# Performance work log

Measured on AMD Instinct MI355X. Metric: run time of the kernel, lower is better.

Reference implementation:

```python
import jax, jax.numpy as jnp
import numpy as np

N_VOCAB_TOTAL = 32064  # n_vocab + n_nts
D_MODEL = 256


def setup_inputs() -> dict:
    key = jax.random.key(0)
    ks = jax.random.split(key, 8)
    d = D_MODEL
    tokens = jax.random.randint(ks[0], (64, 4095), 0, N_VOCAB_TOTAL, dtype=jnp.int32)
    # embedding_tgt: normal with std 1/sqrt(d) (reset_parameters)
    E = jax.random.normal(ks[1], (N_VOCAB_TOTAL, d), dtype=jnp.float32) / jnp.sqrt(jnp.float32(d))
    s_in = 1.0 / np.sqrt(3 * d)
    s_h = 1.0 / np.sqrt(d)
    W_in = jax.random.uniform(ks[2], (d, 3 * d), jnp.float32, -s_in, s_in)  # Linear(3d, d)
    b_in = jax.random.uniform(ks[3], (d,), jnp.float32, -s_in, s_in)
    W1 = jax.random.uniform(ks[4], (d, d), jnp.float32, -s_h, s_h)
    b1 = jax.random.uniform(ks[5], (d,), jnp.float32, -s_h, s_h)
    W2 = jax.random.uniform(ks[6], (d, d), jnp.float32, -s_h, s_h)
    b2 = jax.random.uniform(ks[7], (d,), jnp.float32, -s_h, s_h)
    return {"tokens": tokens, "E": E, "W_in": W_in, "b_in": b_in,
            "W1": W1, "b1": b1, "W2": W2, "b2": b2}


def _bin_agg(roots, left, right, W_in, b_in, W1, b1, W2, b2):
    # skipmlp_binary_agg: root + hidden(inp(cat([root,left,right])))
    # hidden = ELU -> Linear -> ELU -> Linear  (nlayers=2)
    x = jnp.concatenate([roots, left, right], axis=-1)        # [..., 3d]
    h = x @ W_in.T + b_in                                     # inp: Linear(3d, d)
    h = jax.nn.elu(h) @ W1.T + b1
    h = jax.nn.elu(h) @ W2.T + b2
    return roots + h


def reference(tokens, E, W_in, b_in, W1, b1, W2, b2):
    # tokens: [B, N] heap-ordered perfect binary trees, N = 2^(D+1)-1.
    B, N = tokens.shape
    n_leaves = (N + 1) // 2
    emb = E[tokens]                                           # [B, N, d] gather
    cur = emb[:, N - n_leaves:]                               # leaf level, [B, 2^D, d]
    level = n_leaves // 2
    while level >= 1:                                          # fixed D iterations
        roots = emb[:, level - 1: 2 * level - 1]               # [B, level, d]
        left = cur[:, 0::2]
        right = cur[:, 1::2]
        cur = _bin_agg(roots, left, right, W_in, b_in, W1, b1, W2, b2)
        level //= 2
    return cur[:, 0]                                           # [B, d] root embeddings
```

## Files before the change

kernel.cpp:

```cpp
#include <hip/hip_runtime.h>
#include <stdint.h>


typedef __attribute__((ext_vector_type(8))) short short8;
typedef __attribute__((ext_vector_type(4))) float f32x4;

#define XS_STRIDE 264
#define TOK_N 4095

__device__ __forceinline__ unsigned short f32_to_bf16(float f) {
    union { float f; unsigned u; } v; v.f = f;
    return (unsigned short)((v.u + 0x7fffu + ((v.u >> 16) & 1u)) >> 16);
}
__device__ __forceinline__ float bf16_to_f32(unsigned short u) {
    union { unsigned u; float f; } v; v.u = ((unsigned)u) << 16; return v.f;
}

__global__ void convert_f32_bf16(const float* __restrict__ E,
                                 const float* __restrict__ Win,
                                 const float* __restrict__ W1,
                                 const float* __restrict__ W2,
                                 unsigned short* __restrict__ Ebf,
                                 unsigned short* __restrict__ Winbf,
                                 unsigned short* __restrict__ W1bf,
                                 unsigned short* __restrict__ W2bf) {
    const int nE = 32064 * 256, nWin = 256 * 768, nW = 256 * 256;
    const int total4 = (nE + nWin + 2 * nW) >> 2;
    for (int i = blockIdx.x * blockDim.x + threadIdx.x; i < total4;
         i += gridDim.x * blockDim.x) {
        int idx = i << 2;
        const float* src; unsigned short* dst; int off;
        if (idx < nE)                  { src = E;   dst = Ebf;   off = idx; }
        else if (idx < nE + nWin)      { src = Win; dst = Winbf; off = idx - nE; }
        else if (idx < nE + nWin + nW) { src = W1;  dst = W1bf;  off = idx - nE - nWin; }
        else                           { src = W2;  dst = W2bf;  off = idx - nE - nWin - nW; }
        float4 f = *(const float4*)(src + off);
        ushort4 o;
        o.x = f32_to_bf16(f.x); o.y = f32_to_bf16(f.y);
        o.z = f32_to_bf16(f.z); o.w = f32_to_bf16(f.w);
        *(ushort4*)(dst + off) = o;
    }
}

template<int MT>
__global__ __launch_bounds__(256, 4)
void tree_level(const int* __restrict__ tokens,
                const unsigned short* __restrict__ Ebf,
                const unsigned short* __restrict__ Win,
                const unsigned short* __restrict__ W1,
                const unsigned short* __restrict__ W2,
                const float* __restrict__ b_in,
                const float* __restrict__ b1,
                const float* __restrict__ b2,
                const unsigned short* __restrict__ cur_in,
                unsigned short* __restrict__ cur_out,
                float* __restrict__ final_out,
                int L, int logL, int first, int last)
{
    constexpr int R = MT * 16;
    constexpr int GITER = R / 8;
    __shared__ unsigned short Xs[R * XS_STRIDE];

    const int tid  = threadIdx.x;
    const int lane = tid & 63;
    const int wid  = tid >> 6;
    const int l15  = lane & 15;
    const int q    = lane >> 4;
    const int n0   = wid * 64;
    const int blk  = blockIdx.x;
    const int c    = tid & 31;
    const int sub  = tid >> 5;

    auto gsrc = [&](int p, int r) -> const unsigned short* {
        int g = blk * R + r;
        int b = g >> logL;
        int i = g - (b << logL);
        if (p == 0) {
            int tok = tokens[b * TOK_N + (L - 1) + i];
            return Ebf + (size_t)tok * 256;
        } else if (first) {
            int tok = tokens[b * TOK_N + 2047 + 2 * i + (p - 1)];
            return Ebf + (size_t)tok * 256;
        } else {
            return cur_in + ((size_t)b * (2 * L) + 2 * i + (p - 1)) * 256;
        }
    };

    short8 g[GITER];

#pragma unroll
    for (int it = 0; it < GITER; ++it)
        g[it] = *(const short8*)(gsrc(0, it * 8 + sub) + c * 8);
#pragma unroll
    for (int it = 0; it < GITER; ++it)
        *(short8*)(&Xs[(it * 8 + sub) * XS_STRIDE + c * 8]) = g[it];
    __syncthreads();

    f32x4 acc[MT][4];
    float bv[4];
#pragma unroll
    for (int nt = 0; nt < 4; ++nt) bv[nt] = b_in[n0 + nt * 16 + l15];
#pragma unroll
    for (int mt = 0; mt < MT; ++mt)
#pragma unroll
        for (int nt = 0; nt < 4; ++nt)
            acc[mt][nt] = (f32x4){bv[nt], bv[nt], bv[nt], bv[nt]};

    const unsigned short* wbase = Win + q * 8 + (size_t)(n0 + l15) * 768;
    for (int p = 0; p < 3; ++p) {
        const int kbase = p * 256;
        short8 bb[2][4];
#pragma unroll
        for (int k = 0; k < 2; ++k)
#pragma unroll
            for (int nt = 0; nt < 4; ++nt)
                bb[k][nt] = *(const short8*)(wbase + (size_t)(nt * 16) * 768 + kbase + k * 32);
        if (p < 2) {
#pragma unroll
            for (int it = 0; it < GITER; ++it)
                g[it] = *(const short8*)(gsrc(p + 1, it * 8 + sub) + c * 8);
        }
#pragma unroll
        for (int k = 0; k < 8; ++k) {
            short8 a[MT];
#pragma unroll
            for (int mt = 0; mt < MT; ++mt)
                a[mt] = *(const short8*)(&Xs[(mt * 16 + l15) * XS_STRIDE + k * 32 + q * 8]);
#pragma unroll
            for (int mt = 0; mt < MT; ++mt)
#pragma unroll
                for (int nt = 0; nt < 4; ++nt)
                    acc[mt][nt] = __builtin_amdgcn_mfma_f32_16x16x32_bf16(
                        a[mt], bb[k & 1][nt], acc[mt][nt], 0, 0, 0);
            if (k + 2 < 8) {
#pragma unroll
                for (int nt = 0; nt < 4; ++nt)
                    bb[k & 1][nt] = *(const short8*)(wbase + (size_t)(nt * 16) * 768 + kbase + (k + 2) * 32);
            }
        }
        __syncthreads();
        if (p < 2) {
#pragma unroll
            for (int it = 0; it < GITER; ++it)
                *(short8*)(&Xs[(it * 8 + sub) * XS_STRIDE + c * 8]) = g[it];
            __syncthreads();
        }
    }

#pragma unroll
    for (int mt = 0; mt < MT; ++mt)
#pragma unroll
        for (int nt = 0; nt < 4; ++nt)
#pragma unroll
            for (int r = 0; r < 4; ++r) {
                float h = acc[mt][nt][r];
                h = h > 0.f ? h : (__expf(h) - 1.f);
                Xs[(mt * 16 + q * 4 + r) * XS_STRIDE + n0 + nt * 16 + l15] = f32_to_bf16(h);
            }
    __syncthreads();

#pragma unroll
    for (int nt = 0; nt < 4; ++nt) bv[nt] = b1[n0 + nt * 16 + l15];
#pragma unroll
    for (int mt = 0; mt < MT; ++mt)
#pragma unroll
        for (int nt = 0; nt < 4; ++nt)
            acc[mt][nt] = (f32x4){bv[nt], bv[nt], bv[nt], bv[nt]};
    {
        const unsigned short* w1base = W1 + q * 8 + (size_t)(n0 + l15) * 256;
        short8 bb[2][4];
#pragma unroll
        for (int k = 0; k < 2; ++k)
#pragma unroll
            for (int nt = 0; nt < 4; ++nt)
                bb[k][nt] = *(const short8*)(w1base + (size_t)(nt * 16) * 256 + k * 32);
#pragma unroll
        for (int it = 0; it < GITER; ++it)
            g[it] = *(const short8*)(gsrc(0, it * 8 + sub) + c * 8);
#pragma unroll
        for (int k = 0; k < 8; ++k) {
            short8 a[MT];
#pragma unroll
            for (int mt = 0; mt < MT; ++mt)
                a[mt] = *(const short8*)(&Xs[(mt * 16 + l15) * XS_STRIDE + k * 32 + q * 8]);
#pragma unroll
            for (int mt = 0; mt < MT; ++mt)
#pragma unroll
                for (int nt = 0; nt < 4; ++nt)
                    acc[mt][nt] = __builtin_amdgcn_mfma_f32_16x16x32_bf16(
                        a[mt], bb[k & 1][nt], acc[mt][nt], 0, 0, 0);
            if (k + 2 < 8) {
#pragma unroll
                for (int nt = 0; nt < 4; ++nt)
                    bb[k & 1][nt] = *(const short8*)(w1base + (size_t)(nt * 16) * 256 + (k + 2) * 32);
            }
        }
    }
    __syncthreads();

#pragma unroll
    for (int mt = 0; mt < MT; ++mt)
#pragma unroll
        for (int nt = 0; nt < 4; ++nt)
#pragma unroll
            for (int r = 0; r < 4; ++r) {
                float h = acc[mt][nt][r];
                h = h > 0.f ? h : (__expf(h) - 1.f);
                Xs[(mt * 16 + q * 4 + r) * XS_STRIDE + n0 + nt * 16 + l15] = f32_to_bf16(h);
            }
    __syncthreads();

#pragma unroll
    for (int nt = 0; nt < 4; ++nt) bv[nt] = b2[n0 + nt * 16 + l15];
#pragma unroll
    for (int mt = 0; mt < MT; ++mt)
#pragma unroll
        for (int nt = 0; nt < 4; ++nt)
            acc[mt][nt] = (f32x4){bv[nt], bv[nt], bv[nt], bv[nt]};
    {
        const unsigned short* w2base = W2 + q * 8 + (size_t)(n0 + l15) * 256;
        short8 bb[2][4];
#pragma unroll
        for (int k = 0; k < 2; ++k)
#pragma unroll
            for (int nt = 0; nt < 4; ++nt)
                bb[k][nt] = *(const short8*)(w2base + (size_t)(nt * 16) * 256 + k * 32);
#pragma unroll
        for (int k = 0; k < 8; ++k) {
            short8 a[MT];
#pragma unroll
            for (int mt = 0; mt < MT; ++mt)
                a[mt] = *(const short8*)(&Xs[(mt * 16 + l15) * XS_STRIDE + k * 32 + q * 8]);
#pragma unroll
            for (int mt = 0; mt < MT; ++mt)
#pragma unroll
                for (int nt = 0; nt < 4; ++nt)
                    acc[mt][nt] = __builtin_amdgcn_mfma_f32_16x16x32_bf16(
                        a[mt], bb[k & 1][nt], acc[mt][nt], 0, 0, 0);
            if (k + 2 < 8) {
#pragma unroll
                for (int nt = 0; nt < 4; ++nt)
                    bb[k & 1][nt] = *(const short8*)(w2base + (size_t)(nt * 16) * 256 + (k + 2) * 32);
            }
        }
    }
    __syncthreads();
#pragma unroll
    for (int it = 0; it < GITER; ++it)
        *(short8*)(&Xs[(it * 8 + sub) * XS_STRIDE + c * 8]) = g[it];
    __syncthreads();

#pragma unroll
    for (int mt = 0; mt < MT; ++mt)
#pragma unroll
        for (int r = 0; r < 4; ++r) {
            int row = mt * 16 + q * 4 + r;
            int gg  = blk * R + row;
#pragma unroll
            for (int nt = 0; nt < 4; ++nt) {
                int col = n0 + nt * 16 + l15;
                float o = acc[mt][nt][r] + bf16_to_f32(Xs[row * XS_STRIDE + col]);
                if (last) final_out[(size_t)gg * 256 + col] = o;
                else      cur_out[(size_t)gg * 256 + col] = f32_to_bf16(o);
            }
        }
}

extern "C" void kernel_launch(void* const* d_in, const int* in_sizes, int n_in,
                              void* d_out, int out_size, void* d_ws, size_t ws_size,
                              hipStream_t stream) {
    const int*   tokens = (const int*)  d_in[0];
    const float* E      = (const float*)d_in[1];
    const float* W_in   = (const float*)d_in[2];
    const float* b_in   = (const float*)d_in[3];
    const float* W1     = (const float*)d_in[4];
    const float* b1     = (const float*)d_in[5];
    const float* W2     = (const float*)d_in[6];
    const float* b2     = (const float*)d_in[7];
    float* out = (float*)d_out;
    char* ws = (char*)d_ws;

    unsigned short* Ebf   = (unsigned short*)(ws);
    unsigned short* Winbf = (unsigned short*)(ws + 16416768);
    unsigned short* W1bf  = (unsigned short*)(ws + 16809984);
    unsigned short* W2bf  = (unsigned short*)(ws + 16941056);
    unsigned short* curA  = (unsigned short*)(ws + 17072128);
    unsigned short* curB  = (unsigned short*)(ws + 50626560);

    convert_f32_bf16<<<1024, 256, 0, stream>>>(E, W_in, W1, W2,
                                               Ebf, Winbf, W1bf, W2bf);

    const unsigned short* cin = curA;
    unsigned short* cout = curA;
    int first = 1;
    for (int L = 1024; L >= 1; L >>= 1) {
        int logL = 31 - __builtin_clz((unsigned)L);
        int last = (L == 1);
        int MTs = (L >= 512) ? 4 : (L == 256 ? 2 : 1);
        int blocks = (64 * L) / (16 * MTs);
        if (MTs == 4)
            tree_level<4><<<dim3(blocks), dim3(256), 0, stream>>>(
                tokens, Ebf, Winbf, W1bf, W2bf, b_in, b1, b2,
                cin, last ? nullptr : cout, last ? out : nullptr, L, logL, first, last);
        else if (MTs == 2)
            tree_level<2><<<dim3(blocks), dim3(256), 0, stream>>>(
                tokens, Ebf, Winbf, W1bf, W2bf, b_in, b1, b2,
                cin, last ? nullptr : cout, last ? out : nullptr, L, logL, first, last);
        else
            tree_level<1><<<dim3(blocks), dim3(256), 0, stream>>>(
                tokens, Ebf, Winbf, W1bf, W2bf, b_in, b1, b2,
                cin, last ? nullptr : cout, last ? out : nullptr, L, logL, first, last);
        cin = cout;
        cout = (cout == curA) ? curB : curA;
        first = 0;
    }
}
```

Before: 530.7 us.

## Fuse small tree levels into one per-batch tail kernel and refactor GEMM passes

Levels 32 down to 1 now run in a single persistent kernel with one block per batch tree, keeping the previous level in shared memory instead of issuing six tiny launches that round-trip through global memory. The GEMM inner loop moves into a shared helper with a deeper weight prefetch for small tiles, and the next gather is scheduled late inside the K loop. Output writes are staged through shared memory so stores to global are coalesced, and launch bounds drop to 3 blocks per SM. The tail kernel runs only 64 blocks and wastes MFMA work on padded rows when levels are small, so it may leave much of the GPU idle.

```diff
diff --git a/kernel.cpp b/kernel.cpp
--- a/kernel.cpp
+++ b/kernel.cpp
@@ -42,8 +42,41 @@
     }
 }
 
+template<int MT, int DEPTH, int WROW, typename F>
+__device__ __forceinline__ void run_pass(const unsigned short* __restrict__ Xs,
+                                         const unsigned short* __restrict__ wlane,
+                                         int kbase, f32x4 (&acc)[MT][4],
+                                         int l15, int q, F&& late)
+{
+    short8 bb[DEPTH][4];
+#pragma unroll
+    for (int d = 0; d < DEPTH; ++d)
+#pragma unroll
+        for (int nt = 0; nt < 4; ++nt)
+            bb[d][nt] = *(const short8*)(wlane + (size_t)(nt * 16) * WROW + kbase + d * 32);
+#pragma unroll
+    for (int k = 0; k < 8; ++k) {
+        if (k == 6) { __builtin_amdgcn_sched_barrier(0); late(); }
+        short8 a[MT];
+#pragma unroll
+        for (int mt = 0; mt < MT; ++mt)
+            a[mt] = *(const short8*)(&Xs[(mt * 16 + l15) * XS_STRIDE + k * 32 + q * 8]);
+#pragma unroll
+        for (int mt = 0; mt < MT; ++mt)
+#pragma unroll
+            for (int nt = 0; nt < 4; ++nt)
+                acc[mt][nt] = __builtin_amdgcn_mfma_f32_16x16x32_bf16(
+                    a[mt], bb[k % DEPTH][nt], acc[mt][nt], 0, 0, 0);
+        if (k + DEPTH < 8) {
+#pragma unroll
+            for (int nt = 0; nt < 4; ++nt)
+                bb[k % DEPTH][nt] = *(const short8*)(wlane + (size_t)(nt * 16) * WROW + kbase + (k + DEPTH) * 32);
+        }
+    }
+}
+
 template<int MT>
-__global__ __launch_bounds__(256, 4)
+__global__ __launch_bounds__(256, 3)
 void tree_level(const int* __restrict__ tokens,
                 const unsigned short* __restrict__ Ebf,
                 const unsigned short* __restrict__ Win,
@@ -54,11 +87,11 @@
                 const float* __restrict__ b2,
                 const unsigned short* __restrict__ cur_in,
                 unsigned short* __restrict__ cur_out,
-                float* __restrict__ final_out,
-                int L, int logL, int first, int last)
+                int L, int logL, int first)
 {
     constexpr int R = MT * 16;
     constexpr int GITER = R / 8;
+    constexpr int DEPTH = (MT >= 4) ? 2 : 4;
     __shared__ unsigned short Xs[R * XS_STRIDE];
 
     const int tid  = threadIdx.x;
@@ -106,38 +139,15 @@
         for (int nt = 0; nt < 4; ++nt)
             acc[mt][nt] = (f32x4){bv[nt], bv[nt], bv[nt], bv[nt]};
 
-    const unsigned short* wbase = Win + q * 8 + (size_t)(n0 + l15) * 768;
+    const unsigned short* winlane = Win + q * 8 + (size_t)(n0 + l15) * 768;
     for (int p = 0; p < 3; ++p) {
-        const int kbase = p * 256;
-        short8 bb[2][4];
-#pragma unroll
-        for (int k = 0; k < 2; ++k)
-#pragma unroll
-            for (int nt = 0; nt < 4; ++nt)
-                bb[k][nt] = *(const short8*)(wbase + (size_t)(nt * 16) * 768 + kbase + k * 32);
-        if (p < 2) {
-#pragma unroll
-            for (int it = 0; it < GITER; ++it)
-                g[it] = *(const short8*)(gsrc(p + 1, it * 8 + sub) + c * 8);
-        }
-#pragma unroll
-        for (int k = 0; k < 8; ++k) {
-            short8 a[MT];
-#pragma unroll
-            for (int mt = 0; mt < MT; ++mt)
-                a[mt] = *(const short8*)(&Xs[(mt * 16 + l15) * XS_STRIDE + k * 32 + q * 8]);
-#pragma unroll
-            for (int mt = 0; mt < MT; ++mt)
-#pragma unroll
-                for (int nt = 0; nt < 4; ++nt)
-                    acc[mt][nt] = __builtin_amdgcn_mfma_f32_16x16x32_bf16(
-                        a[mt], bb[k & 1][nt], acc[mt][nt], 0, 0, 0);
-            if (k + 2 < 8) {
-#pragma unroll
-                for (int nt = 0; nt < 4; ++nt)
-                    bb[k & 1][nt] = *(const short8*)(wbase + (size_t)(nt * 16) * 768 + kbase + (k + 2) * 32);
+        run_pass<MT, DEPTH, 768>(Xs, winlane, p * 256, acc, l15, q, [&]() {
+            if (p < 2) {
+#pragma unroll
+                for (int it = 0; it < GITER; ++it)
+                    g[it] = *(const short8*)(gsrc(p + 1, it * 8 + sub) + c * 8);
             }
-        }
+        });
         __syncthreads();
         if (p < 2) {
 #pragma unroll
@@ -166,36 +176,8 @@
 #pragma unroll
         for (int nt = 0; nt < 4; ++nt)
             acc[mt][nt] = (f32x4){bv[nt], bv[nt], bv[nt], bv[nt]};
-    {
-        const unsigned short* w1base = W1 + q * 8 + (size_t)(n0 + l15) * 256;
-        short8 bb[2][4];
-#pragma unroll
-        for (int k = 0; k < 2; ++k)
-#pragma unroll
-            for (int nt = 0; nt < 4; ++nt)
-                bb[k][nt] = *(const short8*)(w1base + (size_t)(nt * 16) * 256 + k * 32);
-#pragma unroll
-        for (int it = 0; it < GITER; ++it)
-            g[it] = *(const short8*)(gsrc(0, it * 8 + sub) + c * 8);
-#pragma unroll
-        for (int k = 0; k < 8; ++k) {
-            short8 a[MT];
-#pragma unroll
-            for (int mt = 0; mt < MT; ++mt)
-                a[mt] = *(const short8*)(&Xs[(mt * 16 + l15) * XS_STRIDE + k * 32 + q * 8]);
-#pragma unroll
-            for (int mt = 0; mt < MT; ++mt)
-#pragma unroll
-                for (int nt = 0; nt < 4; ++nt)
-                    acc[mt][nt] = __builtin_amdgcn_mfma_f32_16x16x32_bf16(
-                        a[mt], bb[k & 1][nt], acc[mt][nt], 0, 0, 0);
-            if (k + 2 < 8) {
-#pragma unroll
-                for (int nt = 0; nt < 4; ++nt)
-                    bb[k & 1][nt] = *(const short8*)(w1base + (size_t)(nt * 16) * 256 + (k + 2) * 32);
-            }
-        }
-    }
+    run_pass<MT, DEPTH, 256>(Xs, W1 + q * 8 + (size_t)(n0 + l15) * 256, 0,
+                             acc, l15, q, []() {});
     __syncthreads();
 
 #pragma unroll
@@ -217,34 +199,14 @@
 #pragma unroll
         for (int nt = 0; nt < 4; ++nt)
             acc[mt][nt] = (f32x4){bv[nt], bv[nt], bv[nt], bv[nt]};
-    {
-        const unsigned short* w2base = W2 + q * 8 + (size_t)(n0 + l15) * 256;
-        short8 bb[2][4];
-#pragma unroll
-        for (int k = 0; k < 2; ++k)
-#pragma unroll
-            for (int nt = 0; nt < 4; ++nt)
-                bb[k][nt] = *(const short8*)(w2base + (size_t)(nt * 16) * 256 + k * 32);
-#pragma unroll
-        for (int k = 0; k < 8; ++k) {
-            short8 a[MT];
-#pragma unroll
-            for (int mt = 0; mt < MT; ++mt)
-                a[mt] = *(const short8*)(&Xs[(mt * 16 + l15) * XS_STRIDE + k * 32 + q * 8]);
-#pragma unroll
-            for (int mt = 0; mt < MT; ++mt)
-#pragma unroll
-                for (int nt = 0; nt < 4; ++nt)
-                    acc[mt][nt] = __builtin_amdgcn_mfma_f32_16x16x32_bf16(
-                        a[mt], bb[k & 1][nt], acc[mt][nt], 0, 0, 0);
-            if (k + 2 < 8) {
-#pragma unroll
-                for (int nt = 0; nt < 4; ++nt)
-                    bb[k & 1][nt] = *(const short8*)(w2base + (size_t)(nt * 16) * 256 + (k + 2) * 32);
-            }
-        }
-    }
-    __syncthreads();
+    run_pass<MT, DEPTH, 256>(Xs, W2 + q * 8 + (size_t)(n0 + l15) * 256, 0,
+                             acc, l15, q, [&]() {
+#pragma unroll
+        for (int it = 0; it < GITER; ++it)
+            g[it] = *(const short8*)(gsrc(0, it * 8 + sub) + c * 8);
+    });
+    __syncthreads();
+
 #pragma unroll
     for (int it = 0; it < GITER; ++it)
         *(short8*)(&Xs[(it * 8 + sub) * XS_STRIDE + c * 8]) = g[it];
@@ -253,17 +215,164 @@
 #pragma unroll
     for (int mt = 0; mt < MT; ++mt)
 #pragma unroll
-        for (int r = 0; r < 4; ++r) {
-            int row = mt * 16 + q * 4 + r;
-            int gg  = blk * R + row;
-#pragma unroll
-            for (int nt = 0; nt < 4; ++nt) {
+        for (int nt = 0; nt < 4; ++nt)
+#pragma unroll
+            for (int r = 0; r < 4; ++r) {
+                int row = mt * 16 + q * 4 + r;
                 int col = n0 + nt * 16 + l15;
                 float o = acc[mt][nt][r] + bf16_to_f32(Xs[row * XS_STRIDE + col]);
-                if (last) final_out[(size_t)gg * 256 + col] = o;
-                else      cur_out[(size_t)gg * 256 + col] = f32_to_bf16(o);
+                Xs[row * XS_STRIDE + col] = f32_to_bf16(o);
             }
+    __syncthreads();
+
+#pragma unroll
+    for (int it = 0; it < GITER; ++it)
+        *(short8*)(cur_out + ((size_t)(blk * R + it * 8 + sub)) * 256 + c * 8) =
+            *(const short8*)(&Xs[(it * 8 + sub) * XS_STRIDE + c * 8]);
+}
+
+__global__ __launch_bounds__(256, 2)
+void tree_tail(const int* __restrict__ tokens,
+               const unsigned short* __restrict__ Ebf,
+               const unsigned short* __restrict__ Win,
+               const unsigned short* __restrict__ W1,
+               const unsigned short* __restrict__ W2,
+               const float* __restrict__ b_in,
+               const float* __restrict__ b1,
+               const float* __restrict__ b2,
+               const unsigned short* __restrict__ cur_in,
+               float* __restrict__ out)
+{
+    __shared__ unsigned short prev[64 * 256];
+    __shared__ unsigned short Xs[32 * XS_STRIDE];
+    constexpr int MT = 2, GITER = 4, DEPTH = 4;
+
+    const int b    = blockIdx.x;
+    const int tid  = threadIdx.x;
+    const int lane = tid & 63;
+    const int wid  = tid >> 6;
+    const int l15  = lane & 15;
+    const int q    = lane >> 4;
+    const int n0   = wid * 64;
+    const int c    = tid & 31;
+    const int sub  = tid >> 5;
+
+#pragma unroll
+    for (int it = 0; it < 8; ++it) {
+        int idx = it * 256 + tid;
+        *(short8*)(&prev[idx * 8]) = *(const short8*)(cur_in + (size_t)b * 64 * 256 + idx * 8);
+    }
+    __syncthreads();
+
+    const unsigned short* winlane = Win + q * 8 + (size_t)(n0 + l15) * 768;
+    const unsigned short* w1lane  = W1  + q * 8 + (size_t)(n0 + l15) * 256;
+    const unsigned short* w2lane  = W2  + q * 8 + (size_t)(n0 + l15) * 256;
+
+    f32x4 acc[MT][4];
+    float bv[4];
+    short8 g[GITER];
+
+    for (int L = 32; L >= 1; L >>= 1) {
+#pragma unroll
+        for (int it = 0; it < GITER; ++it) {
+            int r = it * 8 + sub;
+            int i = (r < L) ? r : 0;
+            int tok = tokens[b * TOK_N + (L - 1) + i];
+            g[it] = *(const short8*)(Ebf + (size_t)tok * 256 + c * 8);
         }
+#pragma unroll
+        for (int it = 0; it < GITER; ++it)
+            *(short8*)(&Xs[(it * 8 + sub) * XS_STRIDE + c * 8]) = g[it];
+        __syncthreads();
+
+#pragma unroll
+        for (int nt = 0; nt < 4; ++nt) bv[nt] = b_in[n0 + nt * 16 + l15];
+#pragma unroll
+        for (int mt = 0; mt < MT; ++mt)
+#pragma unroll
+            for (int nt = 0; nt < 4; ++nt)
+                acc[mt][nt] = (f32x4){bv[nt], bv[nt], bv[nt], bv[nt]};
+
+        run_pass<MT, DEPTH, 768>(Xs, winlane, 0, acc, l15, q, []() {});
+        __syncthreads();
+        for (int p = 1; p <= 2; ++p) {
+#pragma unroll
+            for (int it = 0; it < GITER; ++it) {
+                int r = it * 8 + sub;
+                int i = (r < L) ? r : 0;
+                *(short8*)(&Xs[r * XS_STRIDE + c * 8]) =
+                    *(const short8*)(&prev[(2 * i + (p - 1)) * 256 + c * 8]);
+            }
+            __syncthreads();
+            run_pass<MT, DEPTH, 768>(Xs, winlane, p * 256, acc, l15, q, []() {});
+            __syncthreads();
+        }
+
+#pragma unroll
+        for (int mt = 0; mt < MT; ++mt)
+#pragma unroll
+            for (int nt = 0; nt < 4; ++nt)
+#pragma unroll
+                for (int r = 0; r < 4; ++r) {
+                    float h = acc[mt][nt][r];
+                    h = h > 0.f ? h : (__expf(h) - 1.f);
+                    Xs[(mt * 16 + q * 4 + r) * XS_STRIDE + n0 + nt * 16 + l15] = f32_to_bf16(h);
+                }
+        __syncthreads();
+
+#pragma unroll
+        for (int nt = 0; nt < 4; ++nt) bv[nt] = b1[n0 + nt * 16 + l15];
+#pragma unroll
+        for (int mt = 0; mt < MT; ++mt)
+#pragma unroll
+            for (int nt = 0; nt < 4; ++nt)
+                acc[mt][nt] = (f32x4){bv[nt], bv[nt], bv[nt], bv[nt]};
+        run_pass<MT, DEPTH, 256>(Xs, w1lane, 0, acc, l15, q, []() {});
+        __syncthreads();
+
+#pragma unroll
+        for (int mt = 0; mt < MT; ++mt)
+#pragma unroll
+            for (int nt = 0; nt < 4; ++nt)
+#pragma unroll
+                for (int r = 0; r < 4; ++r) {
+                    float h = acc[mt][nt][r];
+                    h = h > 0.f ? h : (__expf(h) - 1.f);
+                    Xs[(mt * 16 + q * 4 + r) * XS_STRIDE + n0 + nt * 16 + l15] = f32_to_bf16(h);
+                }
+        __syncthreads();
+
+#pragma unroll
+        for (int nt = 0; nt < 4; ++nt) bv[nt] = b2[n0 + nt * 16 + l15];
+#pragma unroll
+        for (int mt = 0; mt < MT; ++mt)
+#pragma unroll
+            for (int nt = 0; nt < 4; ++nt)
+                acc[mt][nt] = (f32x4){bv[nt], bv[nt], bv[nt], bv[nt]};
+        run_pass<MT, DEPTH, 256>(Xs, w2lane, 0, acc, l15, q, []() {});
+        __syncthreads();
+
+#pragma unroll
+        for (int it = 0; it < GITER; ++it)
+            *(short8*)(&Xs[(it * 8 + sub) * XS_STRIDE + c * 8]) = g[it];
+        __syncthreads();
+
+#pragma unroll
+        for (int mt = 0; mt < MT; ++mt)
+#pragma unroll
+            for (int nt = 0; nt < 4; ++nt)
+#pragma unroll
+                for (int r = 0; r < 4; ++r) {
+                    int row = mt * 16 + q * 4 + r;
+                    int col = n0 + nt * 16 + l15;
+                    float o = acc[mt][nt][r] + bf16_to_f32(Xs[row * XS_STRIDE + col]);
+                    if (row < L) {
+                        if (L == 1) out[(size_t)b * 256 + col] = o;
+                        else        prev[row * 256 + col] = f32_to_bf16(o);
+                    }
+                }
+        __syncthreads();
+    }
 }
 
 extern "C" void kernel_launch(void* const* d_in, const int* in_sizes, int n_in,
@@ -290,28 +399,26 @@
     convert_f32_bf16<<<1024, 256, 0, stream>>>(E, W_in, W1, W2,
                                                Ebf, Winbf, W1bf, W2bf);
 
-    const unsigned short* cin = curA;
+    const unsigned short* cin = curB;
     unsigned short* cout = curA;
     int first = 1;
-    for (int L = 1024; L >= 1; L >>= 1) {
+    for (int L = 1024; L >= 64; L >>= 1) {
         int logL = 31 - __builtin_clz((unsigned)L);
-        int last = (L == 1);
         int MTs = (L >= 512) ? 4 : (L == 256 ? 2 : 1);
         int blocks = (64 * L) / (16 * MTs);
         if (MTs == 4)
             tree_level<4><<<dim3(blocks), dim3(256), 0, stream>>>(
-                tokens, Ebf, Winbf, W1bf, W2bf, b_in, b1, b2,
-                cin, last ? nullptr : cout, last ? out : nullptr, L, logL, first, last);
+                tokens, Ebf, Winbf, W1bf, W2bf, b_in, b1, b2, cin, cout, L, logL, first);
         else if (MTs == 2)
             tree_level<2><<<dim3(blocks), dim3(256), 0, stream>>>(
-                tokens, Ebf, Winbf, W1bf, W2bf, b_in, b1, b2,
-                cin, last ? nullptr : cout, last ? out : nullptr, L, logL, first, last);
+                tokens, Ebf, Winbf, W1bf, W2bf, b_in, b1, b2, cin, cout, L, logL, first);
         else
             tree_level<1><<<dim3(blocks), dim3(256), 0, stream>>>(
-                tokens, Ebf, Winbf, W1bf, W2bf, b_in, b1, b2,
-                cin, last ? nullptr : cout, last ? out : nullptr, L, logL, first, last);
+                tokens, Ebf, Winbf, W1bf, W2bf, b_in, b1, b2, cin, cout, L, logL, first);
         cin = cout;
         cout = (cout == curA) ? curB : curA;
         first = 0;
     }
-}
+    tree_tail<<<dim3(64), dim3(256), 0, stream>>>(
+        tokens, Ebf, Winbf, W1bf, W2bf, b_in, b1, b2, cin, out);
+}
```

Measured after the change: 558.8 us. 5.3% more time.
